# Kernel tuning notes

Measured on AMD Instinct MI355X. Metric: run time of the kernel, lower is better.

The kernel has to match this reference:

```python
import jax, jax.numpy as jnp
import numpy as np
import math

R = 16            # input_resolution (window side)
N = R * R         # tokens per window
H = 16            # num_heads
D = 32            # head_dim
SCALE = D ** -0.5

def _rel_pos_index(r):
    # Swin-style relative position index, [N, N] int
    coords = np.stack(np.meshgrid(np.arange(r), np.arange(r), indexing='ij'))  # [2,r,r]
    cf = coords.reshape(2, -1)                          # [2, N]
    rel = cf[:, :, None] - cf[:, None, :]               # [2, N, N]
    rel = rel.transpose(1, 2, 0).astype(np.int64)       # [N, N, 2]
    rel[:, :, 0] += r - 1
    rel[:, :, 1] += r - 1
    rel[:, :, 0] *= 2 * r - 1
    return rel.sum(-1)                                  # [N, N]

def _modulation(n, k):
    # cosine-distance modulation matrix, [n*n, n*n]
    idx = np.arange(n * n)
    rr, cc = idx // n, idx % n
    d = np.sqrt((rr[:, None] - rr[None, :]) ** 2 + (cc[:, None] - cc[None, :]) ** 2)
    T = 4 * (n - 1) * math.sqrt(2)
    f = 2 * math.pi / T
    m = np.exp(np.cos(f * d)) / 2
    if k % n == 0:
        k = k - 1
    bound = m[0, k]
    m = np.where(m < bound, 0.0, m)
    return jnp.asarray(m, jnp.float32)

_REL_IDX = jnp.asarray(_rel_pos_index(R))   # [N, N] int
_MOD = _modulation(R, 3 * R)                 # [N, N] float (eval-mode local modulation)

def setup_inputs() -> dict:
    key = jax.random.key(0)
    ks = jax.random.split(key, 6)
    C = H * D
    return {
        'x': jax.random.normal(ks[0], (128, N, C), jnp.float32),
        'qkv_w': jax.random.normal(ks[1], (3 * C, C), jnp.float32) * 0.02,
        'qkv_b': jax.random.normal(ks[2], (3 * C,), jnp.float32) * 0.02,
        'proj_w': jax.random.normal(ks[3], (C, C), jnp.float32) * 0.02,
        'proj_b': jax.random.normal(ks[4], (C,), jnp.float32) * 0.02,
        'rpb_table': jax.random.normal(ks[5], ((2 * R - 1) ** 2, H), jnp.float32) * 0.02,
    }

def reference(x, qkv_w, qkv_b, proj_w, proj_b, rpb_table):
    B, n, C = x.shape
    # qkv projection: torch Linear is x @ W^T + b
    qkv = x @ qkv_w.T + qkv_b                       # [B, N, 3C]
    qkv = qkv.reshape(B, n, 3, H, D)
    q = qkv[:, :, 0].transpose(0, 2, 1, 3) * SCALE  # [B, H, N, D]
    k = qkv[:, :, 1].transpose(0, 2, 1, 3)
    v = qkv[:, :, 2].transpose(0, 2, 1, 3)
    attn = jnp.einsum('bhnd,bhmd->bhnm', q, k)      # [B, H, N, N]
    bias = rpb_table[_REL_IDX]                      # [N, N, H]
    attn = attn + bias.transpose(2, 0, 1)[None]     # + [1, H, N, N]
    attn = jax.nn.softmax(attn, axis=-1)
    attn = attn * _MOD[None, None]                  # local eval-mode modulation
    out = jnp.einsum('bhnm,bhmd->bhnd', attn, v)    # [B, H, N, D]
    out = out.transpose(0, 2, 1, 3).reshape(B, n, C)
    return out @ proj_w.T + proj_b
```

## Files before the change

kernel.cpp:

```cpp
#include <hip/hip_runtime.h>
#include <hip/hip_bf16.h>

typedef unsigned short u16;
typedef unsigned int u32;
typedef __bf16 bf16x8 __attribute__((ext_vector_type(8)));
typedef float f32x4 __attribute__((ext_vector_type(4)));

#define AS1(p) ((const __attribute__((address_space(1))) void*)(p))
#define AS3(p) ((__attribute__((address_space(3))) void*)(p))

#define TOK   256
#define CDIM  512
#define QKVC  1536
#define LOG2E 1.4426950408889634f
#define QSCALE (0.17677669529663687f * 1.4426950408889634f)

__device__ __forceinline__ u16 f2b(float f) {
  unsigned u = __float_as_uint(f);
  unsigned r = (u + 0x7fffu + ((u >> 16) & 1u)) >> 16;
  return (u16)r;
}
__device__ __forceinline__ u16 f2bc(float f) {
  __bf16 h = (__bf16)f;
  u16 u;
  __builtin_memcpy(&u, &h, 2);
  return u;
}
__device__ __forceinline__ float bf_lo(u32 wd) { return __uint_as_float(wd << 16); }
__device__ __forceinline__ float bf_hi(u32 wd) { return __uint_as_float(wd & 0xffff0000u); }
__device__ __forceinline__ float ex2(float x) {
  float r;
  asm("v_exp_f32 %0, %1" : "=v"(r) : "v"(x));
  return r;
}

__global__ __launch_bounds__(256) void cvt_bf16_kernel(const float* __restrict__ in,
                                                       u16* __restrict__ out, int n) {
  int i = (blockIdx.x * 256 + threadIdx.x) * 8;
  if (i >= n) return;
  float4 a = *(const float4*)(in + i);
  float4 b = *(const float4*)(in + i + 4);
  u16 h[8];
  h[0] = f2b(a.x); h[1] = f2b(a.y); h[2] = f2b(a.z); h[3] = f2b(a.w);
  h[4] = f2b(b.x); h[5] = f2b(b.y); h[6] = f2b(b.z); h[7] = f2b(b.w);
  *(uint4*)(out + i) = *(const uint4*)h;
}

__global__ __launch_bounds__(256) void build_bias2_kernel(const float* __restrict__ rpb,
                                                          u16* __restrict__ bias2) {
  int i = blockIdx.x * 256 + threadIdx.x;
  int tr = i & 63, lane = (i >> 6) & 63, rb = (i >> 12) & 15, h = i >> 16;
  int t = tr >> 2, r = tr & 3;
  int n = rb * 16 + (lane & 15);
  int m = t * 16 + (lane >> 4) * 4 + r;
  int idx = ((n >> 4) - (m >> 4) + 15) * 31 + ((n & 15) - (m & 15) + 15);
  bias2[i] = f2b(rpb[idx * 16 + h] * LOG2E);
}

__global__ __launch_bounds__(256) void build_mod2_kernel(u16* __restrict__ mod2) {
  int i = blockIdx.x * 256 + threadIdx.x;
  int tr = i & 63, lane = (i >> 6) & 63, rb = i >> 12;
  int t = tr >> 2, r = tr & 3;
  int n = rb * 16 + (lane & 15);
  int m = t * 16 + (lane >> 4) * 4 + r;
  int dr = (n >> 4) - (m >> 4), dc = (n & 15) - (m & 15);
  int d2 = dr * dr + dc * dc;
  float val = 0.0f;
  if (d2 <= 229) {
    const float fc = 6.2831853071795864f / (60.0f * 1.4142135623730951f);
    val = expf(cosf(fc * sqrtf((float)d2))) * 0.5f;
  }
  mod2[i] = f2b(val);
}

template<int MODE>
__global__ __launch_bounds__(MODE == 0 ? 512 : 256) void gemm_bt(
    const float* __restrict__ Ax, const u16* __restrict__ A,
    const u16* __restrict__ Bt, const float* __restrict__ bvec,
    u16* __restrict__ oq, u16* __restrict__ ok, u16* __restrict__ ov,
    float* __restrict__ of) {
  constexpr int K = 512;
  constexpr int BM = (MODE == 0) ? 256 : 128;
  constexpr int NT = (MODE == 0) ? 512 : 256;
  constexpr int NBN = (MODE == 0) ? 12 : 4;
  constexpr int PER_XCD = (MODE == 0) ? 192 : 128;
  __shared__ __align__(16) u16 SM[(MODE == 0) ? 32768 : 16384];
  u16* As = SM;
  u16* Bs0 = SM + BM * 64;
  u16* Bs1 = (MODE == 0) ? (SM + BM * 64 + 8192) : Bs0;
  const int tid = threadIdx.x, lane = tid & 63, w = tid >> 6;
  const int wr = w >> 1, wc = w & 1, lr = lane & 15, lg = lane >> 4;
  const int logical = (blockIdx.x & 7) * PER_XCD + (blockIdx.x >> 3);
  const int bm = (logical / (2 * NBN)) * 2 + (logical & 1);
  const int bn = (logical % (2 * NBN)) >> 1;
  const u16* Bg = Bt + (size_t)bn * 128 * K;
  f32x4 acc[4][4];
#pragma unroll
  for (int m = 0; m < 4; ++m)
#pragma unroll
    for (int n = 0; n < 4; ++n) acc[m][n] = (f32x4){0.f, 0.f, 0.f, 0.f};

  if (MODE == 0) {
    float4 ar0[4], ar1[4];
#pragma unroll
    for (int it = 0; it < 4; ++it) {
      int chunk = it * NT + tid;
      int r = chunk >> 3, gg = (chunk & 7) ^ (r & 7);
      const float* src = Ax + (size_t)(bm * 256 + r) * K + gg * 8;
      ar0[it] = *(const float4*)src;
      ar1[it] = *(const float4*)(src + 4);
    }
#pragma unroll
    for (int it = 0; it < 2; ++it) {
      int chunk = it * NT + tid;
      int r = chunk >> 3, kcs = (chunk & 7) ^ (r & 7);
      __builtin_amdgcn_global_load_lds(AS1(Bg + (size_t)r * K + kcs * 8),
                                       AS3(Bs0 + chunk * 8), 16, 0, 0);
    }
#pragma unroll 1
    for (int ks = 0; ks < 8; ++ks) {
      const int k0 = ks * 64;
      u16* Bcur = (ks & 1) ? Bs1 : Bs0;
      u16* Bnxt = (ks & 1) ? Bs0 : Bs1;
#pragma unroll
      for (int it = 0; it < 4; ++it) {
        int chunk = it * NT + tid;
        u16 hb[8];
        hb[0] = f2bc(ar0[it].x); hb[1] = f2bc(ar0[it].y);
        hb[2] = f2bc(ar0[it].z); hb[3] = f2bc(ar0[it].w);
        hb[4] = f2bc(ar1[it].x); hb[5] = f2bc(ar1[it].y);
        hb[6] = f2bc(ar1[it].z); hb[7] = f2bc(ar1[it].w);
        *(uint4*)(As + chunk * 8) = *(const uint4*)hb;
      }
      __syncthreads();
      if (ks < 7) {
#pragma unroll
        for (int it = 0; it < 2; ++it) {
          int chunk = it * NT + tid;
          int r = chunk >> 3, kcs = (chunk & 7) ^ (r & 7);
          __builtin_amdgcn_global_load_lds(AS1(Bg + (size_t)r * K + k0 + 64 + kcs * 8),
                                           AS3(Bnxt + chunk * 8), 16, 0, 0);
        }
#pragma unroll
        for (int it = 0; it < 4; ++it) {
          int chunk = it * NT + tid;
          int r = chunk >> 3, gg = (chunk & 7) ^ (r & 7);
          const float* src = Ax + (size_t)(bm * 256 + r) * K + k0 + 64 + gg * 8;
          ar0[it] = *(const float4*)src;
          ar1[it] = *(const float4*)(src + 4);
        }
      }
#pragma unroll
      for (int kk = 0; kk < 2; ++kk) {
        bf16x8 a[4], b[4];
#pragma unroll
        for (int m = 0; m < 4; ++m) {
          int ar = wr * 64 + m * 16 + lr;
          a[m] = *(const bf16x8*)&As[ar * 64 + (((kk * 4 + lg) ^ (lr & 7)) << 3)];
        }
#pragma unroll
        for (int n = 0; n < 4; ++n) {
          int br = wc * 64 + n * 16 + lr;
          b[n] = *(const bf16x8*)&Bcur[br * 64 + (((kk * 4 + lg) ^ (lr & 7)) << 3)];
        }
#pragma unroll
        for (int m = 0; m < 4; ++m)
#pragma unroll
          for (int n = 0; n < 4; ++n)
            acc[m][n] = __builtin_amdgcn_mfma_f32_16x16x32_bf16(a[m], b[n], acc[m][n], 0, 0, 0);
      }
      __syncthreads();
    }
  } else {
    const u16* Ag = A + (size_t)bm * 128 * K;
    for (int k0 = 0; k0 < K; k0 += 64) {
#pragma unroll
      for (int it = 0; it < 4; ++it) {
        int chunk = it * NT + tid;
        int r = chunk >> 3, kcs = (chunk & 7) ^ (r & 7);
        __builtin_amdgcn_global_load_lds(AS1(Ag + (size_t)r * K + k0 + kcs * 8),
                                         AS3(As + chunk * 8), 16, 0, 0);
        __builtin_amdgcn_global_load_lds(AS1(Bg + (size_t)r * K + k0 + kcs * 8),
                                         AS3(Bs0 + chunk * 8), 16, 0, 0);
      }
      __syncthreads();
#pragma unroll
      for (int kk = 0; kk < 2; ++kk) {
        bf16x8 a[4], b[4];
#pragma unroll
        for (int m = 0; m < 4; ++m) {
          int ar = wr * 64 + m * 16 + lr;
          a[m] = *(const bf16x8*)&As[ar * 64 + (((kk * 4 + lg) ^ (lr & 7)) << 3)];
        }
#pragma unroll
        for (int n = 0; n < 4; ++n) {
          int br = wc * 64 + n * 16 + lr;
          b[n] = *(const bf16x8*)&Bs0[br * 64 + (((kk * 4 + lg) ^ (lr & 7)) << 3)];
        }
#pragma unroll
        for (int m = 0; m < 4; ++m)
#pragma unroll
          for (int n = 0; n < 4; ++n)
            acc[m][n] = __builtin_amdgcn_mfma_f32_16x16x32_bf16(a[m], b[n], acc[m][n], 0, 0, 0);
      }
      __syncthreads();
    }
  }

  if (MODE == 1) {
#pragma unroll
    for (int m = 0; m < 4; ++m)
#pragma unroll
      for (int n = 0; n < 4; ++n)
#pragma unroll
        for (int r = 0; r < 4; ++r) {
          int row = bm * BM + wr * 64 + m * 16 + lg * 4 + r;
          int col = bn * 128 + wc * 64 + n * 16 + lr;
          of[(size_t)row * CDIM + col] = acc[m][n][r] + bvec[col];
        }
    return;
  }

  const int typ = bn >> 2;
  const int col0 = bn * 128 + wc * 64;
  const int row0 = bm * 256 + wr * 64;
  char* Tb = (char*)SM + w * 8192;

#pragma unroll
  for (int n = 0; n < 4; ++n) {
    float bv = bvec[col0 + n * 16 + lr];
#pragma unroll
    for (int m = 0; m < 4; ++m)
#pragma unroll
      for (int r = 0; r < 4; ++r) {
        float v = acc[m][n][r] + bv;
        if (typ == 0) v *= QSCALE;
        int row_l, col_l;
        if (typ < 2) { row_l = m * 16 + lg * 4 + r; col_l = n * 16 + lr; }
        else         { row_l = n * 16 + lr;         col_l = m * 16 + lg * 4 + r; }
        int byte = row_l * 128 + ((((col_l >> 3) ^ (row_l & 7)) << 4) | ((col_l & 7) << 1));
        *(u16*)(Tb + byte) = f2b(v);
      }
  }
  asm volatile("" ::: "memory");
  if (typ < 2) {
    int tok = row0 + lane;
    int tokb = tok >> 8;
    u16* obase = (typ == 0) ? oq : ok;
#pragma unroll
    for (int G = 0; G < 8; ++G) {
      int hl = G >> 2, q = G & 3;
      uint4 v = *(const uint4*)(Tb + lane * 128 + ((G ^ (lane & 7)) << 4));
      int hh = ((col0 >> 5) & 15) + hl;
      size_t a = ((((size_t)tokb * 16 + hh) * 16 + ((tok >> 4) & 15)) * 64 +
                  ((tok & 15) | (q << 4))) * 8;
      *(uint4*)(obase + a) = v;
    }
  } else {
    int tl0 = row0 & 255, tokb = row0 >> 8;
    int hl = lane >> 5, t = (lane >> 3) & 3, c = lane & 7;
    int hh = ((col0 >> 5) & 15) + hl;
#pragma unroll
    for (int i = 0; i < 8; ++i) {
      int d = i * 4 + t;
      uint4 v = *(const uint4*)(Tb + (hl * 32 + d) * 128 + (c << 4));
      size_t a = (((size_t)tokb * 16 + hh) * 32 + d) * 256 + tl0 + c * 8;
      *(uint4*)(ov + a) = v;
    }
  }
}

__global__ __launch_bounds__(512, 4) void attn_kernel(const u16* __restrict__ qfrag,
                                                      const u16* __restrict__ kfrag,
                                                      const u16* __restrict__ vsw,
                                                      const u16* __restrict__ bias2,
                                                      const u16* __restrict__ mod2,
                                                      u16* __restrict__ attnout) {
  __shared__ __align__(16) u16 SM[24576];
  const int logical = (blockIdx.x & 7) * 512 + (blockIdx.x >> 3);
  const int h = logical >> 8;
  const int b = (logical >> 1) & 127;
  const int qpair = logical & 1;
  const int tid = threadIdx.x, lane = tid & 63, w = tid >> 6;
  const int lr = lane & 15, lg = lane >> 4;
  const int rb = qpair * 8 + w;
  const int bhid = b * 16 + h;

  const u16* kg = kfrag + (size_t)bhid * 8192;
  const u16* vg = vsw + (size_t)bhid * 8192;
#pragma unroll
  for (int it = 0; it < 2; ++it) {
    __builtin_amdgcn_global_load_lds(AS1(kg + (it * 512 + tid) * 8),
                                     AS3(SM + (it * 512 + tid) * 8), 16, 0, 0);
    __builtin_amdgcn_global_load_lds(AS1(vg + (it * 512 + tid) * 8),
                                     AS3(SM + 8192 + (it * 512 + tid) * 8), 16, 0, 0);
  }
  bf16x8 qf = *(const bf16x8*)(qfrag + ((size_t)bhid * 16 + rb) * 512 + lane * 8);
  __syncthreads();

  const u16* bias_base = bias2 + (((size_t)h * 16 + rb) * 64 + lane) * 64;
  const u16* mod_base  = mod2 + ((size_t)rb * 64 + lane) * 64;
  char* Pbase = (char*)SM + 32768 + w * 2048;
  const char* Vb = (const char*)(SM + 8192);

  f32x4 s[16];
#pragma unroll
  for (int q = 0; q < 4; ++q) {
    u32 bw8[8];
    {
      const uint4* bp = (const uint4*)(bias_base + q * 16);
      *(uint4*)&bw8[0] = bp[0]; *(uint4*)&bw8[4] = bp[1];
    }
#pragma unroll
    for (int tl = 0; tl < 4; ++tl) {
      int t = q * 4 + tl;
      bf16x8 kf = *(const bf16x8*)(SM + (t * 64 + lane) * 8);
      f32x4 c;
      c[0] = bf_lo(bw8[tl * 2]);     c[1] = bf_hi(bw8[tl * 2]);
      c[2] = bf_lo(bw8[tl * 2 + 1]); c[3] = bf_hi(bw8[tl * 2 + 1]);
      s[t] = __builtin_amdgcn_mfma_f32_16x16x32_bf16(kf, qf, c, 0, 0, 0);
    }
  }

  float mr0 = s[0][0], mr1 = s[0][1], mr2 = s[0][2], mr3 = s[0][3];
#pragma unroll
  for (int t = 1; t < 16; ++t) {
    mr0 = fmaxf(mr0, s[t][0]); mr1 = fmaxf(mr1, s[t][1]);
    mr2 = fmaxf(mr2, s[t][2]); mr3 = fmaxf(mr3, s[t][3]);
  }
  float mx = fmaxf(fmaxf(mr0, mr1), fmaxf(mr2, mr3));
  mx = fmaxf(mx, __shfl_xor(mx, 16, 64));
  mx = fmaxf(mx, __shfl_xor(mx, 32, 64));
  float s0 = 0.f, s1 = 0.f, s2 = 0.f, s3 = 0.f;
#pragma unroll
  for (int t = 0; t < 16; ++t) {
    s[t][0] = ex2(s[t][0] - mx); s0 += s[t][0];
    s[t][1] = ex2(s[t][1] - mx); s1 += s[t][1];
    s[t][2] = ex2(s[t][2] - mx); s2 += s[t][2];
    s[t][3] = ex2(s[t][3] - mx); s3 += s[t][3];
  }
  float sm = (s0 + s1) + (s2 + s3);
  sm += __shfl_xor(sm, 16, 64);
  sm += __shfl_xor(sm, 32, 64);
  sm = __builtin_amdgcn_rcpf(sm);

  f32x4 o0 = (f32x4){0.f, 0.f, 0.f, 0.f};
  f32x4 o1 = (f32x4){0.f, 0.f, 0.f, 0.f};
#pragma unroll
  for (int q = 0; q < 4; ++q) {
    u32 mw8[8];
    {
      const uint4* mp = (const uint4*)(mod_base + q * 16);
      *(uint4*)&mw8[0] = mp[0]; *(uint4*)&mw8[4] = mp[1];
    }
#pragma unroll
    for (int tl = 0; tl < 4; ++tl) {
      int t = q * 4 + tl;
      u16 pk[4];
#pragma unroll
      for (int r = 0; r < 4; ++r) {
        u32 wd = mw8[tl * 2 + (r >> 1)];
        float mf = (r & 1) ? bf_hi(wd) : bf_lo(wd);
        pk[r] = f2bc(s[t][r] * sm * mf);
      }
      int hi2 = (t * 2 + (lg >> 1)) & 3;
      *(uint2*)(Pbase + ((t >> 1) & 1) * 1024 + ((hi2 << 4) | lr) * 16 + (lg & 1) * 8)
          = *(const uint2*)pk;
    }
    asm volatile("" ::: "memory");
#pragma unroll
    for (int kl = 0; kl < 2; ++kl) {
      bf16x8 pa = *(const bf16x8*)(Pbase + kl * 1024 + lane * 16);
      int cv = ((q * 2 + kl) * 4 + lg) ^ (lr & 7);
      bf16x8 v0 = *(const bf16x8*)(Vb + lr * 512 + cv * 16);
      bf16x8 v1 = *(const bf16x8*)(Vb + (16 + lr) * 512 + cv * 16);
      o0 = __builtin_amdgcn_mfma_f32_16x16x32_bf16(pa, v0, o0, 0, 0, 0);
      o1 = __builtin_amdgcn_mfma_f32_16x16x32_bf16(pa, v1, o1, 0, 0, 0);
    }
    asm volatile("" ::: "memory");
  }

  u16* orow = attnout + (size_t)(b * TOK + rb * 16) * CDIM + h * 32;
#pragma unroll
  for (int r = 0; r < 4; ++r) {
    orow[(size_t)(lg * 4 + r) * CDIM + lr] = f2bc(o0[r]);
    orow[(size_t)(lg * 4 + r) * CDIM + 16 + lr] = f2bc(o1[r]);
  }
}

extern "C" void kernel_launch(void* const* d_in, const int* in_sizes, int n_in,
                              void* d_out, int out_size, void* d_ws, size_t ws_size,
                              hipStream_t stream) {
  const float* x      = (const float*)d_in[0];
  const float* qkv_w  = (const float*)d_in[1];
  const float* qkv_b  = (const float*)d_in[2];
  const float* proj_w = (const float*)d_in[3];
  const float* proj_b = (const float*)d_in[4];
  const float* rpb    = (const float*)d_in[5];

  char* ws = (char*)d_ws;
  u16* qkvwb  = (u16*)(ws + 33554432);
  u16* projwb = (u16*)(ws + 35127296);
  u16* qfrag  = (u16*)(ws + 35651584);
  u16* kfrag  = (u16*)(ws + 69206016);
  u16* vswb   = (u16*)(ws + 102760448);
  u16* attnb  = (u16*)(ws + 136314880);
  u16* bias2  = (u16*)(ws + 169869312);
  u16* mod2   = (u16*)(ws + 171966464);

  cvt_bf16_kernel<<<384, 256, 0, stream>>>(qkv_w, qkvwb, 1536 * 512);
  cvt_bf16_kernel<<<128, 256, 0, stream>>>(proj_w, projwb, 512 * 512);
  build_bias2_kernel<<<4096, 256, 0, stream>>>(rpb, bias2);
  build_mod2_kernel<<<256, 256, 0, stream>>>(mod2);

  gemm_bt<0><<<1536, 512, 0, stream>>>(x, nullptr, qkvwb, qkv_b,
                                       qfrag, kfrag, vswb, nullptr);
  attn_kernel<<<4096, 512, 0, stream>>>(qfrag, kfrag, vswb, bias2, mod2, attnb);
  gemm_bt<1><<<1024, 256, 0, stream>>>(nullptr, attnb, projwb, proj_b,
                                       nullptr, nullptr, nullptr, (float*)d_out);
}
```

Before: 227.2 us.

## Retile QKV GEMM to 128-row blocks with double-buffered A and B

Shrinks the QKV projection tile from 256x128 with 512 threads to 128x128 with 256 threads and doubles the grid. The fp32-to-bf16 conversion of A now goes into a second LDS buffer after the MFMA block instead of before the barrier, so conversion overlaps compute. The aim is better occupancy (two blocks per CU) and latency hiding. The cost is less reuse of the weight tile and more block scheduling overhead.

New measurement: 240.2 us. 5.7% more time.

```diff
diff --git a/kernel.cpp b/kernel.cpp
--- a/kernel.cpp
+++ b/kernel.cpp
@@ -74,20 +74,19 @@
 }
 
 template<int MODE>
-__global__ __launch_bounds__(MODE == 0 ? 512 : 256) void gemm_bt(
+__global__ __launch_bounds__(256, 2) void gemm_bt(
     const float* __restrict__ Ax, const u16* __restrict__ A,
     const u16* __restrict__ Bt, const float* __restrict__ bvec,
     u16* __restrict__ oq, u16* __restrict__ ok, u16* __restrict__ ov,
     float* __restrict__ of) {
   constexpr int K = 512;
-  constexpr int BM = (MODE == 0) ? 256 : 128;
-  constexpr int NT = (MODE == 0) ? 512 : 256;
   constexpr int NBN = (MODE == 0) ? 12 : 4;
-  constexpr int PER_XCD = (MODE == 0) ? 192 : 128;
+  constexpr int PER_XCD = (MODE == 0) ? 384 : 128;
   __shared__ __align__(16) u16 SM[(MODE == 0) ? 32768 : 16384];
-  u16* As = SM;
-  u16* Bs0 = SM + BM * 64;
-  u16* Bs1 = (MODE == 0) ? (SM + BM * 64 + 8192) : Bs0;
+  u16* As0 = SM;
+  u16* Bs0 = SM + 8192;
+  u16* As1 = (MODE == 0) ? (SM + 16384) : As0;
+  u16* Bs1 = (MODE == 0) ? (SM + 24576) : Bs0;
   const int tid = threadIdx.x, lane = tid & 63, w = tid >> 6;
   const int wr = w >> 1, wc = w & 1, lr = lane & 15, lg = lane >> 4;
   const int logical = (blockIdx.x & 7) * PER_XCD + (blockIdx.x >> 3);
@@ -101,53 +100,57 @@
     for (int n = 0; n < 4; ++n) acc[m][n] = (f32x4){0.f, 0.f, 0.f, 0.f};
 
   if (MODE == 0) {
-    float4 ar0[4], ar1[4];
+    const float* Abase = Ax + (size_t)(bm * 128) * K;
+    float4 pa0[4], pa1[4];
 #pragma unroll
     for (int it = 0; it < 4; ++it) {
-      int chunk = it * NT + tid;
+      int chunk = it * 256 + tid;
       int r = chunk >> 3, gg = (chunk & 7) ^ (r & 7);
-      const float* src = Ax + (size_t)(bm * 256 + r) * K + gg * 8;
-      ar0[it] = *(const float4*)src;
-      ar1[it] = *(const float4*)(src + 4);
-    }
-#pragma unroll
-    for (int it = 0; it < 2; ++it) {
-      int chunk = it * NT + tid;
+      const float* src = Abase + (size_t)r * K + gg * 8;
+      pa0[it] = *(const float4*)src;
+      pa1[it] = *(const float4*)(src + 4);
+    }
+#pragma unroll
+    for (int it = 0; it < 4; ++it) {
+      int chunk = it * 256 + tid;
       int r = chunk >> 3, kcs = (chunk & 7) ^ (r & 7);
       __builtin_amdgcn_global_load_lds(AS1(Bg + (size_t)r * K + kcs * 8),
                                        AS3(Bs0 + chunk * 8), 16, 0, 0);
     }
-#pragma unroll 1
+#pragma unroll
+    for (int it = 0; it < 4; ++it) {
+      int chunk = it * 256 + tid;
+      u16 hb[8];
+      hb[0] = f2bc(pa0[it].x); hb[1] = f2bc(pa0[it].y);
+      hb[2] = f2bc(pa0[it].z); hb[3] = f2bc(pa0[it].w);
+      hb[4] = f2bc(pa1[it].x); hb[5] = f2bc(pa1[it].y);
+      hb[6] = f2bc(pa1[it].z); hb[7] = f2bc(pa1[it].w);
+      *(uint4*)(As0 + chunk * 8) = *(const uint4*)hb;
+    }
+    __syncthreads();
+
+#pragma unroll
     for (int ks = 0; ks < 8; ++ks) {
-      const int k0 = ks * 64;
-      u16* Bcur = (ks & 1) ? Bs1 : Bs0;
-      u16* Bnxt = (ks & 1) ? Bs0 : Bs1;
-#pragma unroll
-      for (int it = 0; it < 4; ++it) {
-        int chunk = it * NT + tid;
-        u16 hb[8];
-        hb[0] = f2bc(ar0[it].x); hb[1] = f2bc(ar0[it].y);
-        hb[2] = f2bc(ar0[it].z); hb[3] = f2bc(ar0[it].w);
-        hb[4] = f2bc(ar1[it].x); hb[5] = f2bc(ar1[it].y);
-        hb[6] = f2bc(ar1[it].z); hb[7] = f2bc(ar1[it].w);
-        *(uint4*)(As + chunk * 8) = *(const uint4*)hb;
-      }
-      __syncthreads();
+      u16* Ac = (ks & 1) ? As1 : As0;
+      u16* Bc = (ks & 1) ? Bs1 : Bs0;
+      u16* An = (ks & 1) ? As0 : As1;
+      u16* Bn = (ks & 1) ? Bs0 : Bs1;
       if (ks < 7) {
-#pragma unroll
-        for (int it = 0; it < 2; ++it) {
-          int chunk = it * NT + tid;
+        const int kn = (ks + 1) * 64;
+#pragma unroll
+        for (int it = 0; it < 4; ++it) {
+          int chunk = it * 256 + tid;
           int r = chunk >> 3, kcs = (chunk & 7) ^ (r & 7);
-          __builtin_amdgcn_global_load_lds(AS1(Bg + (size_t)r * K + k0 + 64 + kcs * 8),
-                                           AS3(Bnxt + chunk * 8), 16, 0, 0);
+          __builtin_amdgcn_global_load_lds(AS1(Bg + (size_t)r * K + kn + kcs * 8),
+                                           AS3(Bn + chunk * 8), 16, 0, 0);
         }
 #pragma unroll
         for (int it = 0; it < 4; ++it) {
-          int chunk = it * NT + tid;
+          int chunk = it * 256 + tid;
           int r = chunk >> 3, gg = (chunk & 7) ^ (r & 7);
-          const float* src = Ax + (size_t)(bm * 256 + r) * K + k0 + 64 + gg * 8;
-          ar0[it] = *(const float4*)src;
-          ar1[it] = *(const float4*)(src + 4);
+          const float* src = Abase + (size_t)r * K + kn + gg * 8;
+          pa0[it] = *(const float4*)src;
+          pa1[it] = *(const float4*)(src + 4);
         }
       }
 #pragma unroll
@@ -156,18 +159,30 @@
 #pragma unroll
         for (int m = 0; m < 4; ++m) {
           int ar = wr * 64 + m * 16 + lr;
-          a[m] = *(const bf16x8*)&As[ar * 64 + (((kk * 4 + lg) ^ (lr & 7)) << 3)];
+          a[m] = *(const bf16x8*)&Ac[ar * 64 + (((kk * 4 + lg) ^ (lr & 7)) << 3)];
         }
 #pragma unroll
         for (int n = 0; n < 4; ++n) {
           int br = wc * 64 + n * 16 + lr;
-          b[n] = *(const bf16x8*)&Bcur[br * 64 + (((kk * 4 + lg) ^ (lr & 7)) << 3)];
+          b[n] = *(const bf16x8*)&Bc[br * 64 + (((kk * 4 + lg) ^ (lr & 7)) << 3)];
         }
 #pragma unroll
         for (int m = 0; m < 4; ++m)
 #pragma unroll
           for (int n = 0; n < 4; ++n)
             acc[m][n] = __builtin_amdgcn_mfma_f32_16x16x32_bf16(a[m], b[n], acc[m][n], 0, 0, 0);
+      }
+      if (ks < 7) {
+#pragma unroll
+        for (int it = 0; it < 4; ++it) {
+          int chunk = it * 256 + tid;
+          u16 hb[8];
+          hb[0] = f2bc(pa0[it].x); hb[1] = f2bc(pa0[it].y);
+          hb[2] = f2bc(pa0[it].z); hb[3] = f2bc(pa0[it].w);
+          hb[4] = f2bc(pa1[it].x); hb[5] = f2bc(pa1[it].y);
+          hb[6] = f2bc(pa1[it].z); hb[7] = f2bc(pa1[it].w);
+          *(uint4*)(An + chunk * 8) = *(const uint4*)hb;
+        }
       }
       __syncthreads();
     }
@@ -176,10 +191,10 @@
     for (int k0 = 0; k0 < K; k0 += 64) {
 #pragma unroll
       for (int it = 0; it < 4; ++it) {
-        int chunk = it * NT + tid;
+        int chunk = it * 256 + tid;
         int r = chunk >> 3, kcs = (chunk & 7) ^ (r & 7);
         __builtin_amdgcn_global_load_lds(AS1(Ag + (size_t)r * K + k0 + kcs * 8),
-                                         AS3(As + chunk * 8), 16, 0, 0);
+                                         AS3(As0 + chunk * 8), 16, 0, 0);
         __builtin_amdgcn_global_load_lds(AS1(Bg + (size_t)r * K + k0 + kcs * 8),
                                          AS3(Bs0 + chunk * 8), 16, 0, 0);
       }
@@ -190,7 +205,7 @@
 #pragma unroll
         for (int m = 0; m < 4; ++m) {
           int ar = wr * 64 + m * 16 + lr;
-          a[m] = *(const bf16x8*)&As[ar * 64 + (((kk * 4 + lg) ^ (lr & 7)) << 3)];
+          a[m] = *(const bf16x8*)&As0[ar * 64 + (((kk * 4 + lg) ^ (lr & 7)) << 3)];
         }
 #pragma unroll
         for (int n = 0; n < 4; ++n) {
@@ -214,7 +229,7 @@
       for (int n = 0; n < 4; ++n)
 #pragma unroll
         for (int r = 0; r < 4; ++r) {
-          int row = bm * BM + wr * 64 + m * 16 + lg * 4 + r;
+          int row = bm * 128 + wr * 64 + m * 16 + lg * 4 + r;
           int col = bn * 128 + wc * 64 + n * 16 + lr;
           of[(size_t)row * CDIM + col] = acc[m][n][r] + bvec[col];
         }
@@ -223,7 +238,7 @@
 
   const int typ = bn >> 2;
   const int col0 = bn * 128 + wc * 64;
-  const int row0 = bm * 256 + wr * 64;
+  const int row0 = bm * 128 + wr * 64;
   char* Tb = (char*)SM + w * 8192;
 
 #pragma unroll
@@ -413,7 +428,7 @@
   build_bias2_kernel<<<4096, 256, 0, stream>>>(rpb, bias2);
   build_mod2_kernel<<<256, 256, 0, stream>>>(mod2);
 
-  gemm_bt<0><<<1536, 512, 0, stream>>>(x, nullptr, qkvwb, qkv_b,
+  gemm_bt<0><<<3072, 256, 0, stream>>>(x, nullptr, qkvwb, qkv_b,
                                        qfrag, kfrag, vswb, nullptr);
   attn_kernel<<<4096, 512, 0, stream>>>(qfrag, kfrag, vswb, bias2, mod2, attnb);
   gemm_bt<1><<<1024, 256, 0, stream>>>(nullptr, attnb, projwb, proj_b,
```
